# Kernel tuning notes

Hardware: AMD Instinct MI355X
Metric: run time of the kernel (lower is better)

Reference implementation:

```python
import jax, jax.numpy as jnp
import numpy as np

FREQ_DIM = 64
BLOCK_DIM = 64
N = 256          # lattice sites
CH = 6           # channel_num -> block diagonals at offsets -1, 0, +1
S = 2 * 16 + CH - 2   # seq_num = 36
BS = 4           # block_size (kron of two 2x2 matrices)
HID = 128
EPS = 1e-5
B = 32

_e = np.eye(2)
_sx = np.array([[0., 1.], [1., 0.]])
_siy = np.array([[0., 1.], [-1., 0.]])
_sz = np.array([[1., 0.], [0., -1.]])
_p = [_e, _sx, _siy, _sz]
KRONS = jnp.asarray(np.stack([np.kron(_p[a], _p[b]) for a in range(4) for b in range(4)]).astype(np.float32))  # (16,4,4)
Z1 = KRONS[12]  # kron(sigma_z, I) used for interaction blocks ('z1')


def _bn(h, g, b):
    # BatchNorm1d in training mode: biased batch statistics over axis 0
    mu = h.mean(axis=0)
    v = h.var(axis=0)
    return g * (h - mu) / jnp.sqrt(v + EPS) + b


def _mlp(x, Win, bin_, Wmid, bmid, Wout, bout, gamma, beta):
    # depth-4 MLP: Lin+ReLU, then (BN,Lin,ReLU) x2, then BN,Lin,ReLU
    h = jax.nn.relu(x @ Win + bin_)
    for i in range(Wmid.shape[0]):
        h = jax.nn.relu(_bn(h, gamma[i], beta[i]) @ Wmid[i] + bmid[i])
    return jax.nn.relu(_bn(h, gamma[-1], beta[-1]) @ Wout + bout)


def _lstm(xs, h0, c0, Wih, Whh, bih, bhh):
    # xs: (B, T, S); torch gate order i, f, g, o
    def step(carry, x_t):
        h, c = carry
        gates = x_t @ Wih.T + h @ Whh.T + (bih + bhh)
        i, f, g, o = jnp.split(gates, 4, axis=-1)
        c = jax.nn.sigmoid(f) * c + jax.nn.sigmoid(i) * jnp.tanh(g)
        h = jax.nn.sigmoid(o) * jnp.tanh(c)
        return (h, c), h
    _, hs = jax.lax.scan(step, (h0, c0), jnp.swapaxes(xs, 0, 1))
    return jnp.swapaxes(hs, 0, 1)


def setup_inputs() -> dict:
    key = jax.random.key(0)
    ks = iter(jax.random.split(key, 48))
    def w(shape, s=0.05):
        return jax.random.normal(next(ks), shape, dtype=jnp.float32) * s
    d = {
        'x': w((B, FREQ_DIM + BLOCK_DIM), 1.0),
        'fd_Win': w((FREQ_DIM, HID)), 'fd_bin': w((HID,)),
        'fd_Wmid': w((2, HID, HID)), 'fd_bmid': w((2, HID)),
        'fd_Wout': w((HID, S)), 'fd_bout': w((S,)),
        'fd_gamma': jnp.ones((3, HID), jnp.float32), 'fd_beta': jnp.zeros((3, HID), jnp.float32),
        'bd_Win': w((BLOCK_DIM, HID)), 'bd_bin': w((HID,)),
        'bd_Wmid': w((2, HID, HID)), 'bd_bmid': w((2, HID)),
        'bd_Wout': w((HID, S)), 'bd_bout': w((S,)),
        'bd_gamma': jnp.ones((3, HID), jnp.float32), 'bd_beta': jnp.zeros((3, HID), jnp.float32),
        'sc_Win': w((S, 1, HID)), 'sc_bin': w((S, HID)),
        'sc_Wmid': w((S, 2, HID, HID)), 'sc_bmid': w((S, 2, HID)),
        'sc_Wout': w((S, HID, N)), 'sc_bout': w((S, N)),
        'sc_gamma': jnp.ones((S, 3, HID), jnp.float32), 'sc_beta': jnp.zeros((S, 3, HID), jnp.float32),
        'lstm_Wih': w((4 * S, S)), 'lstm_Whh': w((4 * S, S)),
        'lstm_bih': w((4 * S,)), 'lstm_bhh': w((4 * S,)),
        'mix_W': w((S, 2 * S)), 'mix_b': w((S,)),
    }
    return d


def reference(x, fd_Win, fd_bin, fd_Wmid, fd_bmid, fd_Wout, fd_bout, fd_gamma, fd_beta,
              bd_Win, bd_bin, bd_Wmid, bd_bmid, bd_Wout, bd_bout, bd_gamma, bd_beta,
              sc_Win, sc_bin, sc_Wmid, sc_bmid, sc_Wout, sc_bout, sc_gamma, sc_beta,
              lstm_Wih, lstm_Whh, lstm_bih, lstm_bhh, mix_W, mix_b):
    Bsz = x.shape[0]
    block = _mlp(x[:, FREQ_DIM:], bd_Win, bd_bin, bd_Wmid, bd_bmid, bd_Wout, bd_bout, bd_gamma, bd_beta)  # (B,S)
    freq = _mlp(x[:, :FREQ_DIM], fd_Win, fd_bin, fd_Wmid, fd_bmid, fd_Wout, fd_bout, fd_gamma, fd_beta)   # (B,S)
    # S independent scalar->N MLPs, batched with vmap over the stacked params
    sc = jax.vmap(_mlp)(freq.T[:, :, None], sc_Win, sc_bin, sc_Wmid, sc_bmid,
                        sc_Wout, sc_bout, sc_gamma, sc_beta)  # (S,B,N)
    freq_seq = jnp.cos(sc).transpose(1, 2, 0)   # (B,N,S)
    seq = _lstm(freq_seq, block, jnp.zeros_like(block), lstm_Wih, lstm_Whh, lstm_bih, lstm_bhh)  # (B,N,S)
    block_seq = jnp.concatenate([jnp.broadcast_to(block[:, :, None], (Bsz, S, N)),
                                 jnp.swapaxes(seq, 1, 2)], axis=1)  # (B,2S,N)
    # 1x1 Conv2d == channel mixing matmul
    mixed = jnp.einsum('bcn,oc->bon', block_seq, mix_W) + mix_b[None, :, None]  # (B,S,N)
    inter = mixed[:, :CH - 2]                          # (B,CH-2,N)
    onsite = mixed[:, CH - 2:].reshape(Bsz, 2, 16, N)  # (B,2,16,N)
    H_int = jnp.einsum('bcn,ij->bcnij', inter, Z1)         # (B,CH-2,N,4,4)
    H_os = jnp.einsum('bgkn,kij->bgnij', onsite, KRONS)    # (B,2,N,4,4) summed over 16 pairs
    half = (CH - 2) // 2
    strips = jnp.concatenate([H_int[:, :half], H_os, H_int[:, half:]], axis=1)  # (B,CH,N,4,4)
    strips = strips.reshape(Bsz, CH // 2, 2, N, BS, BS)
    # banded block assembly: strip i lives on block-diagonal offset i - (CH//2)//2
    grid = jnp.zeros((Bsz, 2, N, N, BS, BS), dtype=x.dtype)
    for i in range(CH // 2):
        o = i - (CH // 2) // 2
        rows = jnp.arange(N - abs(o)) + max(0, -o)
        cols = rows + o
        grid = grid.at[:, :, rows, cols].set(strips[:, i][:, :, rows])
    matrix = grid.transpose(0, 1, 2, 4, 3, 5).reshape(Bsz, 2, N * BS, N * BS)
    return matrix
```

## Files before the change

### kernel.cpp

```cpp
#include <hip/hip_runtime.h>
#include <math.h>

#define EPSF 1e-5f
typedef __attribute__((ext_vector_type(2))) float f32x2;
typedef __attribute__((ext_vector_type(4))) float f32x4;

__device__ __forceinline__ float sigf(float x) { return 1.f / (1.f + __expf(-x)); }
__device__ __forceinline__ float tanhf_fast(float x) { return 1.f - 2.f / (__expf(2.f * x) + 1.f); }
__device__ __forceinline__ float rdlane(float v, int k) {
    return __int_as_float(__builtin_amdgcn_readlane(__float_as_int(v), k));
}

__device__ __forceinline__ float pauliv(int p, int r, int c) {
    switch (p) {
        case 0: return (r == c) ? 1.f : 0.f;
        case 1: return (r != c) ? 1.f : 0.f;
        case 2: return (r == 0 && c == 1) ? 1.f : ((r == 1 && c == 0) ? -1.f : 0.f);
        default: return (r == c) ? ((r == 0) ? 1.f : -1.f) : 0.f;
    }
}

__device__ void mlp64_body(const float* __restrict__ xin,
                           const float* __restrict__ Win,
                           const float* __restrict__ bin_,
                           const float* __restrict__ Wmid,
                           const float* __restrict__ bmid,
                           const float* __restrict__ Wout,
                           const float* __restrict__ bout,
                           const float* __restrict__ gamma,
                           const float* __restrict__ beta,
                           float* __restrict__ out)
{
    __shared__ float sX[2048];
    __shared__ float sA[4096];
    __shared__ float sB[4096];
    __shared__ float sMu[128], sRs[128];
    int tid = threadIdx.x;

    for (int idx = tid; idx < 2048; idx += 1024) {
        int b = idx >> 6, c = idx & 63;
        sX[idx] = xin[b * 128 + c];
    }
    __syncthreads();

    for (int idx = tid; idx < 4096; idx += 1024) {
        int b = idx >> 7, j = idx & 127;
        float acc = bin_[j];
        for (int c = 0; c < 64; ++c) acc = fmaf(sX[b * 64 + c], Win[c * 128 + j], acc);
        sA[idx] = fmaxf(acc, 0.f);
    }
    __syncthreads();

    float* cur = sA;
    float* nxt = sB;
    for (int l = 0; l < 3; ++l) {
        if (tid < 128) {
            float s = 0.f, s2 = 0.f;
            for (int b = 0; b < 32; ++b) {
                float v = cur[b * 128 + tid];
                s += v; s2 += v * v;
            }
            float mu = s * (1.f / 32.f);
            float var = s2 * (1.f / 32.f) - mu * mu;
            sMu[tid] = mu;
            sRs[tid] = rsqrtf(var + EPSF);
        }
        __syncthreads();
        for (int idx = tid; idx < 4096; idx += 1024) {
            int j = idx & 127;
            cur[idx] = gamma[l * 128 + j] * (cur[idx] - sMu[j]) * sRs[j] + beta[l * 128 + j];
        }
        __syncthreads();
        if (l < 2) {
            for (int idx = tid; idx < 4096; idx += 1024) {
                int b = idx >> 7, j = idx & 127;
                float acc = bmid[l * 128 + j];
                for (int c = 0; c < 128; ++c)
                    acc = fmaf(cur[b * 128 + c], Wmid[(l * 128 + c) * 128 + j], acc);
                nxt[idx] = fmaxf(acc, 0.f);
            }
            __syncthreads();
            float* t = cur; cur = nxt; nxt = t;
        } else {
            for (int idx = tid; idx < 1152; idx += 1024) {
                int b = idx / 36, j = idx - b * 36;
                float acc = bout[j];
                for (int c = 0; c < 128; ++c)
                    acc = fmaf(cur[b * 128 + c], Wout[c * 36 + j], acc);
                out[idx] = fmaxf(acc, 0.f);
            }
        }
    }
}

__global__ __launch_bounds__(1024) void k_mlp2(
    const float* __restrict__ x,
    const float* fdWin, const float* fdbin, const float* fdWmid, const float* fdbmid,
    const float* fdWout, const float* fdbout, const float* fdg, const float* fdbt,
    const float* bdWin, const float* bdbin, const float* bdWmid, const float* bdbmid,
    const float* bdWout, const float* bdbout, const float* bdg, const float* bdbt,
    float* freq, float* blk)
{
    if (blockIdx.x == 0)
        mlp64_body(x + 64, bdWin, bdbin, bdWmid, bdbmid, bdWout, bdbout, bdg, bdbt, blk);
    else
        mlp64_body(x, fdWin, fdbin, fdWmid, fdbmid, fdWout, fdbout, fdg, fdbt, freq);
}

__global__ __launch_bounds__(512) void k_sc1(
    const float* __restrict__ freq,
    const float* __restrict__ Win,
    const float* __restrict__ bin_,
    const float* __restrict__ Wmid,
    const float* __restrict__ bmid,
    const float* __restrict__ gamma,
    const float* __restrict__ beta,
    float* __restrict__ actW)
{
    int s = blockIdx.x, tid = threadIdx.x;
    __shared__ float sA[4096];
    __shared__ float sB[4096];
    __shared__ float sMu[128], sRs[128];
    const float* Wm = Wmid + (size_t)s * 2 * 128 * 128;
    const float* gm = gamma + s * 3 * 128;
    const float* bt = beta + s * 3 * 128;

    for (int idx = tid; idx < 4096; idx += 512) {
        int b = idx >> 7, j = idx & 127;
        float acc = fmaf(freq[b * 36 + s], Win[s * 128 + j], bin_[s * 128 + j]);
        sA[idx] = fmaxf(acc, 0.f);
    }
    __syncthreads();

    float* cur = sA;
    float* nxt = sB;
    for (int l = 0; l < 3; ++l) {
        if (tid < 128) {
            float sm = 0.f, s2 = 0.f;
            for (int b = 0; b < 32; ++b) {
                float v = cur[b * 128 + tid];
                sm += v; s2 += v * v;
            }
            float mu = sm * (1.f / 32.f);
            float var = s2 * (1.f / 32.f) - mu * mu;
            sMu[tid] = mu;
            sRs[tid] = rsqrtf(var + EPSF);
        }
        __syncthreads();
        for (int idx = tid; idx < 4096; idx += 512) {
            int j = idx & 127;
            cur[idx] = gm[l * 128 + j] * (cur[idx] - sMu[j]) * sRs[j] + bt[l * 128 + j];
        }
        __syncthreads();
        if (l < 2) {
            int jj = tid & 127, bb = tid >> 7;
            float acc[8];
            #pragma unroll
            for (int k = 0; k < 8; ++k) acc[k] = bmid[(s * 2 + l) * 128 + jj];
            for (int c = 0; c < 128; ++c) {
                float w = Wm[(l * 128 + c) * 128 + jj];
                #pragma unroll
                for (int k = 0; k < 8; ++k)
                    acc[k] = fmaf(cur[(bb + 4 * k) * 128 + c], w, acc[k]);
            }
            __syncthreads();
            #pragma unroll
            for (int k = 0; k < 8; ++k) nxt[(bb + 4 * k) * 128 + jj] = fmaxf(acc[k], 0.f);
            __syncthreads();
            float* t = cur; cur = nxt; nxt = t;
        } else {
            for (int idx = tid; idx < 4096; idx += 512)
                actW[(size_t)s * 4096 + idx] = cur[idx];
        }
    }
}

__global__ __launch_bounds__(512) void k_sc2(
    const float* __restrict__ actW,
    const float* __restrict__ Wout,
    const float* __restrict__ bout,
    float* __restrict__ fseq2)
{
    int bidx = blockIdx.x;
    int s = bidx >> 2, q = bidx & 3;
    int tid = threadIdx.x;
    __shared__ float sAct[4096];
    for (int idx = tid; idx < 4096; idx += 512)
        sAct[idx] = actW[(size_t)s * 4096 + idx];
    __syncthreads();

    int nn = (tid & 63) + q * 64;
    int bb = tid >> 6;
    const float* Wo = Wout + (size_t)s * 128 * 256;
    float acc[4];
    #pragma unroll
    for (int k = 0; k < 4; ++k) acc[k] = bout[s * 256 + nn];
    #pragma unroll 4
    for (int c = 0; c < 128; ++c) {
        float w = Wo[c * 256 + nn];
        #pragma unroll
        for (int k = 0; k < 4; ++k)
            acc[k] = fmaf(sAct[(bb + 8 * k) * 128 + c], w, acc[k]);
    }
    #pragma unroll
    for (int k = 0; k < 4; ++k) {
        float v = fmaxf(acc[k], 0.f);
        fseq2[((size_t)s * 32 + bb + 8 * k) * 256 + nn] = __cosf(v);
    }
}

__global__ __launch_bounds__(512) void k_xg(
    const float* __restrict__ fseq2, const float* __restrict__ Wih,
    const float* __restrict__ bih, const float* __restrict__ bhh,
    float* __restrict__ Xg)
{
    int t = blockIdx.x, tid = threadIdx.x;
    __shared__ float sF[1152];
    __shared__ float sWt[36 * 144];
    for (int idx = tid; idx < 1152; idx += 512) {
        int s = idx >> 5, b = idx & 31;
        sF[b * 36 + s] = fseq2[(size_t)idx * 256 + t];
    }
    for (int idx = tid; idx < 5184; idx += 512) {
        int j = idx / 36, s = idx - j * 36;
        sWt[s * 144 + j] = Wih[idx];
    }
    __syncthreads();
    for (int idx = tid; idx < 4608; idx += 512) {
        int b = idx / 144, j = idx - b * 144;
        int g = j / 36, u = j - g * 36;
        float acc = bih[j] + bhh[j];
        #pragma unroll
        for (int s = 0; s < 36; ++s)
            acc = fmaf(sF[b * 36 + s], sWt[s * 144 + j], acc);
        Xg[(((size_t)b * 256 + t) * 36 + u) * 4 + g] = acc;
    }
}

#define PF 8
#define NZBLK 4032
__global__ __launch_bounds__(128) void k_lstm_zero(
    const float* __restrict__ Xg,
    const float* __restrict__ blk,
    const float* __restrict__ Whh,
    float* __restrict__ hseq2,
    float* __restrict__ out, long total4)
{
    if (blockIdx.x >= 32) {
        f32x4* o = (f32x4*)out;
        f32x4 z = f32x4{0.f, 0.f, 0.f, 0.f};
        long start = (long)(blockIdx.x - 32) * 128 + threadIdx.x;
        long stride = (long)NZBLK * 128;
        for (long i = start; i < total4; i += stride) o[i] = z;
        return;
    }

    __shared__ f32x2 sEx[2][2][40];
    int b = blockIdx.x;
    int wid = threadIdx.x >> 6;
    int lane = threadIdx.x & 63;
    int uu = lane < 36 ? lane : 35;
    bool active = lane < 36;

    f32x2 w2[36];
    {
        const float* wA = Whh + (size_t)(wid * 72 + uu) * 36;
        const float* wB = Whh + (size_t)(wid * 72 + 36 + uu) * 36;
        #pragma unroll
        for (int k = 0; k < 36; ++k) w2[k] = f32x2{wA[k], wB[k]};
    }

    float hv = blk[b * 36 + uu];
    float c = 0.f;
    const f32x2* xb2 = (const f32x2*)(Xg + (size_t)b * 256 * 144);
    float* hout = hseq2 + (size_t)b * 256 * 36;

    f32x2 pipe[PF];
    #pragma unroll
    for (int i = 0; i < PF; ++i) pipe[i] = xb2[(i * 36 + uu) * 2 + wid];

    #pragma unroll 8
    for (int t = 0; t < 256; ++t) {
        f32x2 acc0 = pipe[t & (PF - 1)];
        if (t + PF < 256) pipe[t & (PF - 1)] = xb2[((t + PF) * 36 + uu) * 2 + wid];

        f32x2 acc1 = f32x2{0.f, 0.f}, acc2 = f32x2{0.f, 0.f}, acc3 = f32x2{0.f, 0.f};
        #pragma unroll
        for (int k = 0; k < 36; k += 4) {
            float h0 = rdlane(hv, k),     h1 = rdlane(hv, k + 1);
            float h2 = rdlane(hv, k + 2), h3 = rdlane(hv, k + 3);
            acc0 = __builtin_elementwise_fma(w2[k],     f32x2{h0, h0}, acc0);
            acc1 = __builtin_elementwise_fma(w2[k + 1], f32x2{h1, h1}, acc1);
            acc2 = __builtin_elementwise_fma(w2[k + 2], f32x2{h2, h2}, acc2);
            acc3 = __builtin_elementwise_fma(w2[k + 3], f32x2{h3, h3}, acc3);
        }
        f32x2 a = (acc0 + acc1) + (acc2 + acc3);

        f32x2 mypair;
        if (wid == 0) mypair = f32x2{sigf(a.x), sigf(a.y)};
        else          mypair = f32x2{tanhf_fast(a.x), sigf(a.y)};
        if (active) sEx[t & 1][wid][uu] = mypair;
        __syncthreads();
        f32x2 other = sEx[t & 1][wid ^ 1][uu];
        f32x2 ivfv = (wid == 0) ? mypair : other;
        f32x2 gvov = (wid == 0) ? other : mypair;
        c = fmaf(ivfv.y, c, ivfv.x * gvov.x);
        hv = gvov.y * tanhf_fast(c);
        if (wid == 0 && active) hout[t * 36 + uu] = hv;
    }
}

__global__ __launch_bounds__(256) void k_mixed(
    const float* __restrict__ blk, const float* __restrict__ hseq2,
    const float* __restrict__ mixW, const float* __restrict__ mixb,
    float* __restrict__ mixed)
{
    int bq = blockIdx.x;
    int b = bq >> 2, oq = bq & 3;
    int tid = threadIdx.x;
    __shared__ float sH[256 * 37];
    __shared__ float sW[9 * 36];
    __shared__ float sBase[9];
    for (int idx = tid; idx < 9216; idx += 256) {
        int t = idx / 36, u = idx - t * 36;
        sH[t * 37 + u] = hseq2[(size_t)b * 9216 + idx];
    }
    for (int idx = tid; idx < 9 * 36; idx += 256) {
        int o = idx / 36, u = idx - o * 36;
        sW[idx] = mixW[(oq * 9 + o) * 72 + 36 + u];
    }
    if (tid < 9) {
        int o = oq * 9 + tid;
        float acc = mixb[o];
        for (int c = 0; c < 36; ++c) acc = fmaf(mixW[o * 72 + c], blk[b * 36 + c], acc);
        sBase[tid] = acc;
    }
    __syncthreads();
    int n = tid;
    #pragma unroll
    for (int o = 0; o < 9; ++o) {
        float acc = sBase[o];
        #pragma unroll
        for (int u = 0; u < 36; ++u)
            acc = fmaf(sW[o * 36 + u], sH[n * 37 + u], acc);
        mixed[((size_t)b * 36 + oq * 9 + o) * 256 + n] = acc;
    }
}

__global__ __launch_bounds__(256) void k_sparse(
    const float* __restrict__ mixed, float* __restrict__ out)
{
    int bg = blockIdx.x;
    int g = bg & 1, b = bg >> 1;
    int n = threadIdx.x;
    const float* mb = mixed + (size_t)b * 36 * 256;
    float vSub = mb[(size_t)g * 256 + n];
    float vSup = mb[(size_t)(2 + g) * 256 + n];
    float ch[16];
    #pragma unroll
    for (int k = 0; k < 16; ++k) ch[k] = mb[(size_t)(4 + 16 * g + k) * 256 + n];
    float d[16];
    #pragma unroll
    for (int e = 0; e < 16; ++e) {
        int r = e >> 2, cc = e & 3;
        float acc = 0.f;
        #pragma unroll
        for (int k = 0; k < 16; ++k) {
            float kv = pauliv(k >> 2, r >> 1, cc >> 1) * pauliv(k & 3, r & 1, cc & 1);
            if (kv == 1.f) acc = acc + ch[k];
            else if (kv == -1.f) acc = acc - ch[k];
        }
        d[e] = acc;
    }

    float* base = out + (size_t)bg * 1024 * 1024;
    #pragma unroll
    for (int r = 0; r < 4; ++r)
        *(f32x4*)(base + (size_t)(4 * n + r) * 1024 + 4 * n) =
            f32x4{d[r * 4 + 0], d[r * 4 + 1], d[r * 4 + 2], d[r * 4 + 3]};
    if (n > 0) {
        #pragma unroll
        for (int r = 0; r < 4; ++r)
            base[(size_t)(4 * n + r) * 1024 + 4 * (n - 1) + r] = (r < 2) ? vSub : -vSub;
    }
    if (n < 255) {
        #pragma unroll
        for (int r = 0; r < 4; ++r)
            base[(size_t)(4 * n + r) * 1024 + 4 * (n + 1) + r] = (r < 2) ? vSup : -vSup;
    }
}

extern "C" void kernel_launch(void* const* d_in, const int* in_sizes, int n_in,
                              void* d_out, int out_size, void* d_ws, size_t ws_size,
                              hipStream_t stream) {
    const float* x      = (const float*)d_in[0];
    const float* fdWin  = (const float*)d_in[1];
    const float* fdbin  = (const float*)d_in[2];
    const float* fdWmid = (const float*)d_in[3];
    const float* fdbmid = (const float*)d_in[4];
    const float* fdWout = (const float*)d_in[5];
    const float* fdbout = (const float*)d_in[6];
    const float* fdg    = (const float*)d_in[7];
    const float* fdbt   = (const float*)d_in[8];
    const float* bdWin  = (const float*)d_in[9];
    const float* bdbin  = (const float*)d_in[10];
    const float* bdWmid = (const float*)d_in[11];
    const float* bdbmid = (const float*)d_in[12];
    const float* bdWout = (const float*)d_in[13];
    const float* bdbout = (const float*)d_in[14];
    const float* bdg    = (const float*)d_in[15];
    const float* bdbt   = (const float*)d_in[16];
    const float* scWin  = (const float*)d_in[17];
    const float* scbin  = (const float*)d_in[18];
    const float* scWmid = (const float*)d_in[19];
    const float* scbmid = (const float*)d_in[20];
    const float* scWout = (const float*)d_in[21];
    const float* scbout = (const float*)d_in[22];
    const float* scg    = (const float*)d_in[23];
    const float* scbt   = (const float*)d_in[24];
    const float* Wih    = (const float*)d_in[25];
    const float* Whh    = (const float*)d_in[26];
    const float* bih    = (const float*)d_in[27];
    const float* bhh    = (const float*)d_in[28];
    const float* mixW   = (const float*)d_in[29];
    const float* mixb   = (const float*)d_in[30];

    float* ws    = (float*)d_ws;
    float* freq  = ws;
    float* blk   = ws + 1152;
    float* fseq2 = ws + 2304;
    float* Xg    = ws + 297216;
    float* hseq2 = ws + 1476864;
    float* mixed = ws + 1771776;
    float* actW  = Xg;

    float* out = (float*)d_out;
    long total4 = (long)out_size / 4;

    k_mlp2<<<2, 1024, 0, stream>>>(x,
        fdWin, fdbin, fdWmid, fdbmid, fdWout, fdbout, fdg, fdbt,
        bdWin, bdbin, bdWmid, bdbmid, bdWout, bdbout, bdg, bdbt,
        freq, blk);
    k_sc1<<<36, 512, 0, stream>>>(freq, scWin, scbin, scWmid, scbmid, scg, scbt, actW);
    k_sc2<<<144, 512, 0, stream>>>(actW, scWout, scbout, fseq2);
    k_xg<<<256, 512, 0, stream>>>(fseq2, Wih, bih, bhh, Xg);
    k_lstm_zero<<<32 + NZBLK, 128, 0, stream>>>(Xg, blk, Whh, hseq2, out, total4);
    k_mixed<<<128, 256, 0, stream>>>(blk, hseq2, mixW, mixb, mixed);
    k_sparse<<<64, 256, 0, stream>>>(mixed, out);
}
```

Measured before the change: 326.2 us.

## Fuse LSTM, channel mixing and sparse write; move output zeroing into MLP launch

Zeroing the 256MB output moves from the LSTM launch to the first MLP kernel, which now runs 2046 extra zeroing blocks. The LSTM kernel now keeps its hidden sequence in shared memory and does the 1x1 channel mix and banded block scatter itself, which removes the k_mixed and k_sparse launches and their workspace round-trips. The LSTM step loop is rewritten as macro-unrolled steps with rotating prefetch registers, and the Xg prefetch is added after the gate sum. The risk is that the fused epilogue, with only 32 blocks, runs serially after the recurrence, and that zeroing in the first kernel may not overlap with anything long.

```diff
diff --git a/kernel.cpp b/kernel.cpp
--- a/kernel.cpp
+++ b/kernel.cpp
@@ -93,14 +93,22 @@
     }
 }
 
-__global__ __launch_bounds__(1024) void k_mlp2(
+__global__ __launch_bounds__(1024) void k_mlp2_zero(
     const float* __restrict__ x,
     const float* fdWin, const float* fdbin, const float* fdWmid, const float* fdbmid,
     const float* fdWout, const float* fdbout, const float* fdg, const float* fdbt,
     const float* bdWin, const float* bdbin, const float* bdWmid, const float* bdbmid,
     const float* bdWout, const float* bdbout, const float* bdg, const float* bdbt,
-    float* freq, float* blk)
-{
+    float* freq, float* blk, float* out, long total4)
+{
+    if (blockIdx.x >= 2) {
+        f32x4* o = (f32x4*)out;
+        f32x4 z = f32x4{0.f, 0.f, 0.f, 0.f};
+        long start = (long)(blockIdx.x - 2) * 1024 + threadIdx.x;
+        long stride = (long)2046 * 1024;
+        for (long i = start; i < total4; i += stride) o[i] = z;
+        return;
+    }
     if (blockIdx.x == 0)
         mlp64_body(x + 64, bdWin, bdbin, bdWmid, bdbmid, bdWout, bdbout, bdg, bdbt, blk);
     else
@@ -237,25 +245,46 @@
     }
 }
 
-#define PF 8
-#define NZBLK 4032
-__global__ __launch_bounds__(128) void k_lstm_zero(
+#define LSTM_STEP(I, P) do {                                                  \
+    f32x2 acc0 = f32x2{0.f, 0.f}, acc1 = acc0, acc2 = acc0, acc3 = acc0;      \
+    _Pragma("unroll")                                                         \
+    for (int k = 0; k < 36; k += 4) {                                         \
+        float h0 = rdlane(hv, k),     h1 = rdlane(hv, k + 1);                 \
+        float h2 = rdlane(hv, k + 2), h3 = rdlane(hv, k + 3);                 \
+        acc0 = __builtin_elementwise_fma(w2[k],     f32x2{h0, h0}, acc0);     \
+        acc1 = __builtin_elementwise_fma(w2[k + 1], f32x2{h1, h1}, acc1);     \
+        acc2 = __builtin_elementwise_fma(w2[k + 2], f32x2{h2, h2}, acc2);     \
+        acc3 = __builtin_elementwise_fma(w2[k + 3], f32x2{h3, h3}, acc3);     \
+    }                                                                         \
+    f32x2 a = ((acc0 + acc1) + (acc2 + acc3)) + (P);                          \
+     \
+    (P) = xb2[((tb + (I) + 8) * 36 + uu) * 2 + wid];                          \
+    f32x2 mypair;                                                             \
+    if (wid == 0) mypair = f32x2{sigf(a.x), sigf(a.y)};                       \
+    else          mypair = f32x2{tanhf_fast(a.x), sigf(a.y)};                 \
+    if (active) sEx[(I) & 1][wid][uu] = mypair;                               \
+    __syncthreads();                                                          \
+    f32x2 other = sEx[(I) & 1][wid ^ 1][uu];                                  \
+    f32x2 ivfv = (wid == 0) ? mypair : other;                                 \
+    f32x2 gvov = (wid == 0) ? other : mypair;                                 \
+    c = fmaf(ivfv.y, c, ivfv.x * gvov.x);                                     \
+    hv = gvov.y * tanhf_fast(c);                                              \
+    if (wid == 0 && active) hbuf[(tb + (I)) * 36 + uu] = hv;                  \
+} while (0)
+
+__global__ __launch_bounds__(128) void k_lstm_fused(
     const float* __restrict__ Xg,
     const float* __restrict__ blk,
     const float* __restrict__ Whh,
-    float* __restrict__ hseq2,
-    float* __restrict__ out, long total4)
-{
-    if (blockIdx.x >= 32) {
-        f32x4* o = (f32x4*)out;
-        f32x4 z = f32x4{0.f, 0.f, 0.f, 0.f};
-        long start = (long)(blockIdx.x - 32) * 128 + threadIdx.x;
-        long stride = (long)NZBLK * 128;
-        for (long i = start; i < total4; i += stride) o[i] = z;
-        return;
-    }
-
+    const float* __restrict__ mixW,
+    const float* __restrict__ mixb,
+    float* __restrict__ out)
+{
+    __shared__ float hbuf[256 * 36];
     __shared__ f32x2 sEx[2][2][40];
+    __shared__ float sWmix[36 * 36];
+    __shared__ float sBase[36];
+
     int b = blockIdx.x;
     int wid = threadIdx.x >> 6;
     int lane = threadIdx.x & 63;
@@ -269,124 +298,84 @@
         #pragma unroll
         for (int k = 0; k < 36; ++k) w2[k] = f32x2{wA[k], wB[k]};
     }
+    for (int idx = threadIdx.x; idx < 1296; idx += 128) {
+        int o = idx / 36, u = idx - o * 36;
+        sWmix[idx] = mixW[o * 72 + 36 + u];
+    }
+    if (threadIdx.x < 36) {
+        int o = threadIdx.x;
+        float acc = mixb[o];
+        for (int cc = 0; cc < 36; ++cc) acc = fmaf(mixW[o * 72 + cc], blk[b * 36 + cc], acc);
+        sBase[o] = acc;
+    }
 
     float hv = blk[b * 36 + uu];
     float c = 0.f;
     const f32x2* xb2 = (const f32x2*)(Xg + (size_t)b * 256 * 144);
-    float* hout = hseq2 + (size_t)b * 256 * 36;
-
-    f32x2 pipe[PF];
-    #pragma unroll
-    for (int i = 0; i < PF; ++i) pipe[i] = xb2[(i * 36 + uu) * 2 + wid];
-
-    #pragma unroll 8
-    for (int t = 0; t < 256; ++t) {
-        f32x2 acc0 = pipe[t & (PF - 1)];
-        if (t + PF < 256) pipe[t & (PF - 1)] = xb2[((t + PF) * 36 + uu) * 2 + wid];
-
-        f32x2 acc1 = f32x2{0.f, 0.f}, acc2 = f32x2{0.f, 0.f}, acc3 = f32x2{0.f, 0.f};
-        #pragma unroll
-        for (int k = 0; k < 36; k += 4) {
-            float h0 = rdlane(hv, k),     h1 = rdlane(hv, k + 1);
-            float h2 = rdlane(hv, k + 2), h3 = rdlane(hv, k + 3);
-            acc0 = __builtin_elementwise_fma(w2[k],     f32x2{h0, h0}, acc0);
-            acc1 = __builtin_elementwise_fma(w2[k + 1], f32x2{h1, h1}, acc1);
-            acc2 = __builtin_elementwise_fma(w2[k + 2], f32x2{h2, h2}, acc2);
-            acc3 = __builtin_elementwise_fma(w2[k + 3], f32x2{h3, h3}, acc3);
-        }
-        f32x2 a = (acc0 + acc1) + (acc2 + acc3);
-
-        f32x2 mypair;
-        if (wid == 0) mypair = f32x2{sigf(a.x), sigf(a.y)};
-        else          mypair = f32x2{tanhf_fast(a.x), sigf(a.y)};
-        if (active) sEx[t & 1][wid][uu] = mypair;
-        __syncthreads();
-        f32x2 other = sEx[t & 1][wid ^ 1][uu];
-        f32x2 ivfv = (wid == 0) ? mypair : other;
-        f32x2 gvov = (wid == 0) ? other : mypair;
-        c = fmaf(ivfv.y, c, ivfv.x * gvov.x);
-        hv = gvov.y * tanhf_fast(c);
-        if (wid == 0 && active) hout[t * 36 + uu] = hv;
-    }
-}
-
-__global__ __launch_bounds__(256) void k_mixed(
-    const float* __restrict__ blk, const float* __restrict__ hseq2,
-    const float* __restrict__ mixW, const float* __restrict__ mixb,
-    float* __restrict__ mixed)
-{
-    int bq = blockIdx.x;
-    int b = bq >> 2, oq = bq & 3;
-    int tid = threadIdx.x;
-    __shared__ float sH[256 * 37];
-    __shared__ float sW[9 * 36];
-    __shared__ float sBase[9];
-    for (int idx = tid; idx < 9216; idx += 256) {
-        int t = idx / 36, u = idx - t * 36;
-        sH[t * 37 + u] = hseq2[(size_t)b * 9216 + idx];
-    }
-    for (int idx = tid; idx < 9 * 36; idx += 256) {
-        int o = idx / 36, u = idx - o * 36;
-        sW[idx] = mixW[(oq * 9 + o) * 72 + 36 + u];
-    }
-    if (tid < 9) {
-        int o = oq * 9 + tid;
-        float acc = mixb[o];
-        for (int c = 0; c < 36; ++c) acc = fmaf(mixW[o * 72 + c], blk[b * 36 + c], acc);
-        sBase[tid] = acc;
-    }
-    __syncthreads();
-    int n = tid;
-    #pragma unroll
-    for (int o = 0; o < 9; ++o) {
-        float acc = sBase[o];
-        #pragma unroll
-        for (int u = 0; u < 36; ++u)
-            acc = fmaf(sW[o * 36 + u], sH[n * 37 + u], acc);
-        mixed[((size_t)b * 36 + oq * 9 + o) * 256 + n] = acc;
-    }
-}
-
-__global__ __launch_bounds__(256) void k_sparse(
-    const float* __restrict__ mixed, float* __restrict__ out)
-{
-    int bg = blockIdx.x;
-    int g = bg & 1, b = bg >> 1;
-    int n = threadIdx.x;
-    const float* mb = mixed + (size_t)b * 36 * 256;
-    float vSub = mb[(size_t)g * 256 + n];
-    float vSup = mb[(size_t)(2 + g) * 256 + n];
-    float ch[16];
-    #pragma unroll
-    for (int k = 0; k < 16; ++k) ch[k] = mb[(size_t)(4 + 16 * g + k) * 256 + n];
-    float d[16];
-    #pragma unroll
-    for (int e = 0; e < 16; ++e) {
-        int r = e >> 2, cc = e & 3;
-        float acc = 0.f;
-        #pragma unroll
-        for (int k = 0; k < 16; ++k) {
-            float kv = pauliv(k >> 2, r >> 1, cc >> 1) * pauliv(k & 3, r & 1, cc & 1);
-            if (kv == 1.f) acc = acc + ch[k];
-            else if (kv == -1.f) acc = acc - ch[k];
-        }
-        d[e] = acc;
-    }
-
-    float* base = out + (size_t)bg * 1024 * 1024;
-    #pragma unroll
-    for (int r = 0; r < 4; ++r)
-        *(f32x4*)(base + (size_t)(4 * n + r) * 1024 + 4 * n) =
-            f32x4{d[r * 4 + 0], d[r * 4 + 1], d[r * 4 + 2], d[r * 4 + 3]};
-    if (n > 0) {
-        #pragma unroll
-        for (int r = 0; r < 4; ++r)
-            base[(size_t)(4 * n + r) * 1024 + 4 * (n - 1) + r] = (r < 2) ? vSub : -vSub;
-    }
-    if (n < 255) {
-        #pragma unroll
-        for (int r = 0; r < 4; ++r)
-            base[(size_t)(4 * n + r) * 1024 + 4 * (n + 1) + r] = (r < 2) ? vSup : -vSup;
+
+    f32x2 p0 = xb2[(0 * 36 + uu) * 2 + wid];
+    f32x2 p1 = xb2[(1 * 36 + uu) * 2 + wid];
+    f32x2 p2 = xb2[(2 * 36 + uu) * 2 + wid];
+    f32x2 p3 = xb2[(3 * 36 + uu) * 2 + wid];
+    f32x2 p4 = xb2[(4 * 36 + uu) * 2 + wid];
+    f32x2 p5 = xb2[(5 * 36 + uu) * 2 + wid];
+    f32x2 p6 = xb2[(6 * 36 + uu) * 2 + wid];
+    f32x2 p7 = xb2[(7 * 36 + uu) * 2 + wid];
+    __syncthreads();
+
+    for (int tt = 0; tt < 32; ++tt) {
+        int tb = tt * 8;
+        LSTM_STEP(0, p0); LSTM_STEP(1, p1); LSTM_STEP(2, p2); LSTM_STEP(3, p3);
+        LSTM_STEP(4, p4); LSTM_STEP(5, p5); LSTM_STEP(6, p6); LSTM_STEP(7, p7);
+    }
+    __syncthreads();
+
+    for (int n = threadIdx.x; n < 256; n += 128) {
+        float hreg[36];
+        #pragma unroll
+        for (int u = 0; u < 36; ++u) hreg[u] = hbuf[n * 36 + u];
+        float mv[36];
+        #pragma unroll
+        for (int o = 0; o < 36; ++o) {
+            float acc = sBase[o];
+            #pragma unroll
+            for (int u = 0; u < 36; ++u)
+                acc = fmaf(sWmix[o * 36 + u], hreg[u], acc);
+            mv[o] = acc;
+        }
+        #pragma unroll
+        for (int g = 0; g < 2; ++g) {
+            float vSub = mv[g];
+            float vSup = mv[2 + g];
+            float d[16];
+            #pragma unroll
+            for (int e = 0; e < 16; ++e) {
+                int r = e >> 2, cc2 = e & 3;
+                float acc = 0.f;
+                #pragma unroll
+                for (int k = 0; k < 16; ++k) {
+                    float kv = pauliv(k >> 2, r >> 1, cc2 >> 1) * pauliv(k & 3, r & 1, cc2 & 1);
+                    if (kv == 1.f) acc = acc + mv[4 + 16 * g + k];
+                    else if (kv == -1.f) acc = acc - mv[4 + 16 * g + k];
+                }
+                d[e] = acc;
+            }
+            float* base = out + (size_t)(b * 2 + g) * 1024 * 1024;
+            #pragma unroll
+            for (int r = 0; r < 4; ++r)
+                *(f32x4*)(base + (size_t)(4 * n + r) * 1024 + 4 * n) =
+                    f32x4{d[r * 4 + 0], d[r * 4 + 1], d[r * 4 + 2], d[r * 4 + 3]};
+            if (n > 0) {
+                #pragma unroll
+                for (int r = 0; r < 4; ++r)
+                    base[(size_t)(4 * n + r) * 1024 + 4 * (n - 1) + r] = (r < 2) ? vSub : -vSub;
+            }
+            if (n < 255) {
+                #pragma unroll
+                for (int r = 0; r < 4; ++r)
+                    base[(size_t)(4 * n + r) * 1024 + 4 * (n + 1) + r] = (r < 2) ? vSup : -vSup;
+            }
+        }
     }
 }
 
@@ -430,21 +419,17 @@
     float* blk   = ws + 1152;
     float* fseq2 = ws + 2304;
     float* Xg    = ws + 297216;
-    float* hseq2 = ws + 1476864;
-    float* mixed = ws + 1771776;
     float* actW  = Xg;
 
     float* out = (float*)d_out;
     long total4 = (long)out_size / 4;
 
-    k_mlp2<<<2, 1024, 0, stream>>>(x,
+    k_mlp2_zero<<<2048, 1024, 0, stream>>>(x,
         fdWin, fdbin, fdWmid, fdbmid, fdWout, fdbout, fdg, fdbt,
         bdWin, bdbin, bdWmid, bdbmid, bdWout, bdbout, bdg, bdbt,
-        freq, blk);
+        freq, blk, out, total4);
     k_sc1<<<36, 512, 0, stream>>>(freq, scWin, scbin, scWmid, scbmid, scg, scbt, actW);
     k_sc2<<<144, 512, 0, stream>>>(actW, scWout, scbout, fseq2);
     k_xg<<<256, 512, 0, stream>>>(fseq2, Wih, bih, bhh, Xg);
-    k_lstm_zero<<<32 + NZBLK, 128, 0, stream>>>(Xg, blk, Whh, hseq2, out, total4);
-    k_mixed<<<128, 256, 0, stream>>>(blk, hseq2, mixW, mixb, mixed);
-    k_sparse<<<64, 256, 0, stream>>>(mixed, out);
-}
+    k_lstm_fused<<<32, 128, 0, stream>>>(Xg, blk, Whh, mixW, mixb, out);
+}
```

New measurement: 345.3 us. +5.9%, slower.
